# Performance work log

Hardware: AMD Instinct MI355X
Metric: run time of the kernel (lower is better)

## Reference

```python
import jax, jax.numpy as jnp
import numpy as np

VOCAB = 100000; D = 300; F_NUM = 768
M = 64; N = 16
SURF_L = 4; CTX_L = 50; DOC_L = 100; BODY_L = 200
HEADS = 5


def _conv_relu_avg(x, W, b):
    # x: [B, L, D] tokens-embedded; conv1d (valid) + relu + global avgpool -> [B, F]
    y = jax.lax.conv_general_dilated(x.transpose(0, 2, 1), W, (1,), 'VALID',
                                     dimension_numbers=('NCH', 'OIH', 'NCH'))
    return jax.nn.relu(y + b[None, :, None]).mean(axis=2)


def _mha(q, k, v, num_heads=HEADS):
    # split-head scaled dot-product attention (no learned projections), q:[Lq,D] k,v:[Lk,D]
    Lq, Dm = q.shape
    hd = Dm // num_heads
    qh = q.reshape(Lq, num_heads, hd).transpose(1, 0, 2)
    kh = k.reshape(k.shape[0], num_heads, hd).transpose(1, 0, 2)
    vh = v.reshape(v.shape[0], num_heads, hd).transpose(1, 0, 2)
    att = jax.nn.softmax(jnp.einsum('hqd,hkd->hqk', qh, kh) * (1.0 / np.sqrt(hd)), axis=-1)
    out = jnp.einsum('hqk,hkd->hqd', att, vh)
    return out.transpose(1, 0, 2).reshape(Lq, Dm)


def _cos(a, b, eps=1e-6):
    na = jnp.maximum(jnp.sqrt((a * a).sum(-1)), eps)
    nb = jnp.maximum(jnp.sqrt((b * b).sum(-1)), eps)
    return (a * b).sum(-1) / (na * nb)


def setup_inputs() -> dict:
    key = jax.random.key(0)
    ks = jax.random.split(key, 20)
    inp = {}
    inp['mention_entity'] = jnp.ones((M, N), dtype=jnp.int32)
    inp['m'] = M
    inp['n'] = N
    inp['mention_vec'] = jax.random.randint(ks[0], (M, SURF_L), 0, VOCAB)
    inp['context_vec'] = jax.random.randint(ks[1], (M, CTX_L), 0, VOCAB)
    inp['doc_vec'] = jax.random.randint(ks[2], (DOC_L,), 0, VOCAB)
    inp['title_vec'] = jax.random.normal(ks[3], (N, F_NUM), dtype=jnp.float32)
    inp['body_vec'] = jax.random.randint(ks[4], (N, BODY_L), 0, VOCAB)
    inp['sfeats'] = jnp.zeros((N, 1), dtype=jnp.float32)
    inp['m2c_prior'] = jax.random.uniform(ks[5], (N,), dtype=jnp.float32)
    inp['men2cands'] = jax.random.randint(ks[6], (M, N), 0, VOCAB)
    inp['contexts_ids'] = jax.random.randint(ks[7], (M, CTX_L), 0, VOCAB)
    inp['hand_features'] = jax.random.uniform(ks[8], (N, 1), dtype=jnp.float32)
    inp['bert_doc_vec'] = jax.random.normal(ks[9], (1, F_NUM), dtype=jnp.float32)
    # learned parameters
    inp['embed_table'] = jax.random.normal(ks[10], (VOCAB, D), dtype=jnp.float32) * 0.1
    inp['conv_ms_w'] = jax.random.normal(ks[11], (F_NUM, D, 2), dtype=jnp.float32) * 0.05
    inp['conv_ms_b'] = jnp.zeros((F_NUM,), dtype=jnp.float32)
    inp['conv_mc_w'] = jax.random.normal(ks[12], (F_NUM, D, 5), dtype=jnp.float32) * 0.05
    inp['conv_mc_b'] = jnp.zeros((F_NUM,), dtype=jnp.float32)
    inp['layer_local_w'] = jax.random.normal(ks[13], (7,), dtype=jnp.float32) * 0.3
    inp['layer_local_b'] = jnp.zeros((), dtype=jnp.float32)
    inp['att_w1'] = jax.random.normal(ks[14], (600, 300), dtype=jnp.float32) * 0.05
    inp['att_b1'] = jnp.zeros((300,), dtype=jnp.float32)
    inp['att_w2'] = jax.random.normal(ks[15], (300, 1), dtype=jnp.float32) * 0.05
    inp['att_b2'] = jnp.zeros((), dtype=jnp.float32)
    return inp


def reference(mention_entity, m, n, mention_vec, context_vec, doc_vec, title_vec,
              body_vec, sfeats, m2c_prior, men2cands, contexts_ids, hand_features,
              bert_doc_vec, embed_table, conv_ms_w, conv_ms_b, conv_mc_w, conv_mc_b,
              layer_local_w, layer_local_b, att_w1, att_b1, att_w2, att_b2):
    # per-mention conv features (vectorized over all mentions at once)
    ms = _conv_relu_avg(embed_table[mention_vec], conv_ms_w, conv_ms_b)   # [M,768]
    mc = _conv_relu_avg(embed_table[context_vec], conv_mc_w, conv_mc_b)   # [M,768]
    md = bert_doc_vec[0]                                                  # [768]
    doc_emb = embed_table[doc_vec]                                        # [100,300]
    body_emb = embed_table[body_vec]                                      # [N,200,300]

    # per-candidate cross attention doc<->body, max-pooled over query positions
    att_d_b = jax.vmap(lambda b: _mha(doc_emb, b, b).max(axis=0))(body_emb)          # [N,300]
    att_b_d = jax.vmap(lambda b: _mha(b, doc_emb, doc_emb).max(axis=0))(body_emb)    # [N,300]
    comb = jnp.concatenate([att_d_b, att_b_d], axis=-1)                              # [N,600]
    att_score = jax.nn.sigmoid(jax.nn.relu(comb @ att_w1 + att_b1) @ att_w2 + att_b2)[:, 0]  # [N]

    # LocalCtxAttRanker: candidate-vs-context attention score
    ctx_emb = embed_table[contexts_ids]                                   # [M,50,300]
    cand_emb = embed_table[men2cands]                                     # [M,N,300]
    tok = jnp.einsum('mnd,mtd->mnt', cand_emb, ctx_emb)                   # [M,N,50]
    p = jax.nn.softmax(tok.max(axis=1), axis=-1)                          # [M,50]
    ctxv = jnp.einsum('mt,mtd->md', p, ctx_emb)                           # [M,300]
    local_att = jnp.einsum('mnd,md->mn', cand_emb, ctxv)                  # [M,N]

    cos_st = _cos(ms[:, None, :], title_vec[None, :, :])                  # [M,N]
    cos_dt = _cos(md[None, :], title_vec)                                 # [N]
    cos_ct = _cos(mc[:, None, :], title_vec[None, :, :])                  # [M,N]

    Mm = ms.shape[0]
    bc = lambda v: jnp.broadcast_to(v[None, :], (Mm, v.shape[0]))
    # feature order matches torch.cat((hand_fea, prior, localAtt, attScore, C_score))
    feats = jnp.stack([bc(hand_features[:, 0]), bc(m2c_prior), local_att,
                       bc(att_score), cos_st, bc(cos_dt), cos_ct], axis=-1)  # [M,N,7]
    score = feats @ layer_local_w + layer_local_b                         # [M,N]

    # per-mention standardization (unbiased std, as torch.std), softmax and uniform renorm
    mu = score.mean(axis=1, keepdims=True)
    sd = score.std(axis=1, keepdims=True, ddof=1)
    z = (score - mu) / sd
    sm = jax.nn.softmax(z, axis=1)
    zmin = z.min(axis=1, keepdims=True)
    zmax = z.max(axis=1, keepdims=True)
    u = (z + 1.0 - zmin) / (zmax - zmin)
    u = u / u.sum(axis=1, keepdims=True)
    return (z, sm, u)
```

## Files before the change

kernel.cpp:

```cpp
#include <hip/hip_runtime.h>

#define MM 64
#define NN 16
#define DDIM 300
#define FNUM 768
#define SURF_LL 4
#define CTX_LL 50
#define DOC_LL 100
#define BODY_LL 200
#define NHEADS 5
#define HDIM 60

#define GM 2944
#define GK 1536
#define GN 768

typedef unsigned short u16;
typedef unsigned int u32;
typedef __attribute__((ext_vector_type(8))) short short8;
typedef __attribute__((ext_vector_type(4))) float f32x4;

#define OFF_MSG    0
#define OFF_CTX2G  76800
#define OFF_CANDG  1036800
#define OFF_MS     1344000
#define OFF_MC     1393152
#define OFF_PV0    1442304
#define OFF_PV1    1461504
#define OFF_ASC    1495104
#define OFF_LATT   1495120
#define OFF_ABF    1496144
#define OFF_WTMC   (OFF_ABF + GM*GK/2)
#define OFF_WTMS   (OFF_WTMC + GN*GK/2)

__device__ __forceinline__ u16 f2bf(float x) {
  union { float f; u32 u; } v; v.f = x;
  u32 r = v.u + 0x7FFFu + ((v.u >> 16) & 1u);
  return (u16)(r >> 16);
}

__global__ __launch_bounds__(256) void mega_prep_kernel(
    const float* __restrict__ embed,
    const int* __restrict__ mention_vec,
    const int* __restrict__ context_vec,
    const int* __restrict__ contexts_ids,
    const int* __restrict__ men2cands,
    const float* __restrict__ Wmc,
    const float* __restrict__ Wms,
    float* __restrict__ dst, float* __restrict__ mc,
    float* __restrict__ att_logit,
    u32* __restrict__ Abf, u32* __restrict__ WTmc, float* __restrict__ WTms) {
  int bid = blockIdx.x;
  if (bid < 5250) {
    int e = bid * 256 + threadIdx.x;
    int row = e / DDIM;
    int col = e - row * DDIM;
    int tok;
    if (row < 256)       tok = mention_vec[row];
    else if (row < 3456) tok = contexts_ids[row - 256];
    else                 tok = men2cands[row - 3456];
    dst[e] = embed[(size_t)tok * DDIM + col];
  } else if (bid < 5442) {
    mc[(bid - 5250) * 256 + threadIdx.x] = 0.f;
  } else if (bid == 5442) {
    if (threadIdx.x < NN) att_logit[threadIdx.x] = 0.f;
  } else if (bid < 14275) {
    int idx = (bid - 5443) * 256 + threadIdx.x;
    int r = idx / (GK / 2);
    int kp = idx - r * (GK / 2);
    int k = kp * 2;
    int m = r / 46, t = r - m * 46;
    u32 out = 0;
#pragma unroll
    for (int j = 0; j < 2; j++) {
      int kj = k + j;
      u16 h = 0;
      if (kj < 1500) {
        int tap = kj / 300;
        int d = kj - tap * 300;
        int tok = context_vec[m * CTX_LL + t + tap];
        h = f2bf(embed[(size_t)tok * DDIM + d]);
      }
      out |= (u32)h << (16 * j);
    }
    Abf[idx] = out;
  } else if (bid < 16579) {
    int idx = (bid - 14275) * 256 + threadIdx.x;
    int n = idx / (GK / 2);
    int kp = idx - n * (GK / 2);
    int k = kp * 2;
    u32 out = 0;
#pragma unroll
    for (int j = 0; j < 2; j++) {
      int kj = k + j;
      u16 h = 0;
      if (kj < 1500) {
        int tap = kj / 300;
        int d = kj - tap * 300;
        h = f2bf(Wmc[(size_t)n * 1500 + d * 5 + tap]);
      }
      out |= (u32)h << (16 * j);
    }
    WTmc[idx] = out;
  } else {
    int idx = (bid - 16579) * 256 + threadIdx.x;
    int k = idx / FNUM;
    int f = idx - k * FNUM;
    WTms[idx] = Wms[(size_t)f * 600 + k];
  }
}

__global__ __launch_bounds__(256) void conv_gemm_kernel(
    const u16* __restrict__ A,
    const u16* __restrict__ B,
    const float* __restrict__ bias,
    float* __restrict__ mc) {
  int bn = blockIdx.x, bm = blockIdx.y;
  __shared__ u16 As[64][72];
  __shared__ u16 Bs[64][72];
  int tid = threadIdx.x;
  int w = tid >> 6, lane = tid & 63;
  int wr = w >> 1, wc = w & 1;
  int lg = lane >> 4, lm = lane & 15;
  f32x4 acc[2][2];
#pragma unroll
  for (int i = 0; i < 2; i++)
#pragma unroll
    for (int j = 0; j < 2; j++) acc[i][j] = (f32x4)0.f;
  int c0row = tid >> 3, ck = (tid & 7) * 8;
  const u16* Ag = A + (size_t)(bm * 64) * GK;
  const u16* Bg = B + (size_t)(bn * 64) * GK;
  for (int kt = 0; kt < GK / 64; kt++) {
    int k0 = kt * 64;
    uint4 av0 = *(const uint4*)(Ag + (size_t)c0row * GK + k0 + ck);
    uint4 av1 = *(const uint4*)(Ag + (size_t)(c0row + 32) * GK + k0 + ck);
    uint4 bv0 = *(const uint4*)(Bg + (size_t)c0row * GK + k0 + ck);
    uint4 bv1 = *(const uint4*)(Bg + (size_t)(c0row + 32) * GK + k0 + ck);
    __syncthreads();
    *(uint4*)&As[c0row][ck] = av0;
    *(uint4*)&As[c0row + 32][ck] = av1;
    *(uint4*)&Bs[c0row][ck] = bv0;
    *(uint4*)&Bs[c0row + 32][ck] = bv1;
    __syncthreads();
#pragma unroll
    for (int kk = 0; kk < 2; kk++) {
      short8 af0 = *(const short8*)&As[wr * 32 + lm][kk * 32 + lg * 8];
      short8 af1 = *(const short8*)&As[wr * 32 + 16 + lm][kk * 32 + lg * 8];
      short8 bf0 = *(const short8*)&Bs[wc * 32 + lm][kk * 32 + lg * 8];
      short8 bf1 = *(const short8*)&Bs[wc * 32 + 16 + lm][kk * 32 + lg * 8];
      acc[0][0] = __builtin_amdgcn_mfma_f32_16x16x32_bf16(af0, bf0, acc[0][0], 0, 0, 0);
      acc[0][1] = __builtin_amdgcn_mfma_f32_16x16x32_bf16(af0, bf1, acc[0][1], 0, 0, 0);
      acc[1][0] = __builtin_amdgcn_mfma_f32_16x16x32_bf16(af1, bf0, acc[1][0], 0, 0, 0);
      acc[1][1] = __builtin_amdgcn_mfma_f32_16x16x32_bf16(af1, bf1, acc[1][1], 0, 0, 0);
    }
  }
#pragma unroll
  for (int mf = 0; mf < 2; mf++)
#pragma unroll
    for (int nf = 0; nf < 2; nf++) {
      int col = bn * 64 + wc * 32 + nf * 16 + lm;
      float bb = bias[col];
      int base = bm * 64 + wr * 32 + mf * 16 + lg * 4;
      int mcur = base / 46;
      float s = 0.f;
#pragma unroll
      for (int r = 0; r < 4; r++) {
        float v = fmaxf(acc[mf][nf][r] + bb, 0.f) * (1.0f / 46.0f);
        int mm = (base + r) / 46;
        if (mm != mcur) { atomicAdd(&mc[mcur * FNUM + col], s); s = 0.f; mcur = mm; }
        s += v;
      }
      atomicAdd(&mc[mcur * FNUM + col], s);
    }
}

__device__ __forceinline__ void conv_ms_body(
    const float* __restrict__ msg, const float* __restrict__ WT,
    const float* __restrict__ B, float* __restrict__ ms, int b) {
  int m = b / 3, fi = b - m * 3;
  int f = fi * 256 + threadIdx.x;
  const float* x = msg + m * SURF_LL * DDIM;
  float a0 = 0.f, a1 = 0.f, a2 = 0.f;
  for (int d = 0; d < DDIM; d++) {
    float v0 = x[d], v1 = x[DDIM + d], v2 = x[2 * DDIM + d], v3 = x[3 * DDIM + d];
    float wA = WT[(size_t)(2 * d) * FNUM + f];
    float wB = WT[(size_t)(2 * d + 1) * FNUM + f];
    a0 += v0 * wA + v1 * wB;
    a1 += v1 * wA + v2 * wB;
    a2 += v2 * wA + v3 * wB;
  }
  float bb = B[f];
  float r = fmaxf(a0 + bb, 0.f) + fmaxf(a1 + bb, 0.f) + fmaxf(a2 + bb, 0.f);
  ms[m * FNUM + f] = r * (1.0f / 3.0f);
}

template <int DIR>
__device__ __forceinline__ void scores_pv_body(
    const float* __restrict__ embed, const int* __restrict__ doc_vec,
    const int* __restrict__ body_vec, float* __restrict__ pvp, int b,
    float* __restrict__ smem) {
  constexpr int Lq = DIR ? 200 : 100;
  constexpr int Lk = DIR ? 100 : 200;
  constexpr int KPL = DIR ? 2 : 4;
  constexpr int NQT = DIR ? 7 : 4;
  constexpr int NHALF = DIR ? 1 : 2;
  int qt = b / 80;
  int rem = b - qt * 80;
  int n = rem / 5, h = rem - n * 5;
  const int* qids = DIR ? body_vec + n * BODY_LL : doc_vec;
  const int* kids = DIR ? doc_vec : body_vec + n * BODY_LL;
  float* Ks = smem;
  float* Qs = smem + 12400;
  float* Pl = smem + 12400;
  float* red = smem + 15600;
  for (int idx = threadIdx.x; idx < Lk * 15; idx += 256) {
    int r = idx / 15, c = idx - r * 15;
    float4 v = *(const float4*)(embed + (size_t)kids[r] * DDIM + h * HDIM + c * 4);
    float* dp = Ks + r * 62 + c * 4;
    dp[0] = v.x; dp[1] = v.y; dp[2] = v.z; dp[3] = v.w;
  }
  for (int idx = threadIdx.x; idx < 32 * 15; idx += 256) {
    int r = idx / 15, c = idx - r * 15;
    int q = qt * 32 + r; if (q >= Lq) q = Lq - 1;
    float4 v = *(const float4*)(embed + (size_t)qids[q] * DDIM + h * HDIM + c * 4);
    float* dp = Qs + r * 64 + c * 4;
    dp[0] = v.x; dp[1] = v.y; dp[2] = v.z; dp[3] = v.w;
  }
  __syncthreads();
  int w = threadIdx.x >> 6, lane = threadIdx.x & 63;
  int kcl[KPL];
#pragma unroll
  for (int j = 0; j < KPL; j++) {
    int kk = lane + 64 * j; kcl[j] = (kk < Lk) ? kk : (Lk - 1);
  }
  float acc[8][KPL];
#pragma unroll
  for (int i = 0; i < 8; i++)
#pragma unroll
    for (int j = 0; j < KPL; j++) acc[i][j] = 0.f;
  for (int d = 0; d < HDIM; d += 4) {
    float2 kva[KPL], kvb[KPL];
#pragma unroll
    for (int j = 0; j < KPL; j++) {
      kva[j] = *(const float2*)&Ks[kcl[j] * 62 + d];
      kvb[j] = *(const float2*)&Ks[kcl[j] * 62 + d + 2];
    }
#pragma unroll
    for (int i = 0; i < 8; i++) {
      float4 qv = *(const float4*)&Qs[(w * 8 + i) * 64 + d];
#pragma unroll
      for (int j = 0; j < KPL; j++)
        acc[i][j] += qv.x * kva[j].x + qv.y * kva[j].y +
                     qv.z * kvb[j].x + qv.w * kvb[j].y;
    }
  }
  const float scale = 0.12909944487358056f;
#pragma unroll
  for (int i = 0; i < 8; i++) {
    float mx = -1e30f;
#pragma unroll
    for (int j = 0; j < KPL; j++)
      if (lane + 64 * j < Lk) mx = fmaxf(mx, acc[i][j]);
#pragma unroll
    for (int o = 32; o >= 1; o >>= 1) mx = fmaxf(mx, __shfl_xor(mx, o));
    float mxs = mx * scale;
    float p[KPL];
    float s = 0.f;
#pragma unroll
    for (int j = 0; j < KPL; j++) {
      p[j] = (lane + 64 * j < Lk) ? __expf(acc[i][j] * scale - mxs) : 0.f;
      s += p[j];
    }
#pragma unroll
    for (int o = 32; o >= 1; o >>= 1) s += __shfl_xor(s, o);
    float inv = 1.0f / s;
#pragma unroll
    for (int j = 0; j < KPL; j++) acc[i][j] = p[j] * inv;
  }
  __syncthreads();
  float o[8];
#pragma unroll
  for (int i = 0; i < 8; i++) o[i] = 0.f;
  int dl = (lane < HDIM) ? lane : (HDIM - 1);
#pragma unroll
  for (int half = 0; half < NHALF; half++) {
    int kbase = half * 100;
#pragma unroll
    for (int j = 0; j < KPL; j++) {
      int kk = lane + 64 * j;
      int rel = kk - kbase;
      if (rel >= 0 && rel < 100 && kk < Lk) {
#pragma unroll
        for (int i = 0; i < 8; i++)
          Pl[(w * 8 + i) * 100 + rel] = acc[i][j];
      }
    }
    for (int k4 = 0; k4 < 25; k4++) {
      int k = kbase + k4 * 4;
      float kv0 = Ks[(k + 0) * 62 + dl];
      float kv1 = Ks[(k + 1) * 62 + dl];
      float kv2 = Ks[(k + 2) * 62 + dl];
      float kv3 = Ks[(k + 3) * 62 + dl];
#pragma unroll
      for (int i = 0; i < 8; i++) {
        float4 pq = *(const float4*)&Pl[(w * 8 + i) * 100 + k4 * 4];
        o[i] += pq.x * kv0 + pq.y * kv1 + pq.z * kv2 + pq.w * kv3;
      }
    }
  }
  float omax = -1e30f;
#pragma unroll
  for (int i = 0; i < 8; i++) {
    int q = qt * 32 + w * 8 + i;
    if (q < Lq) omax = fmaxf(omax, o[i]);
  }
  red[w * 64 + lane] = omax;
  __syncthreads();
  if (threadIdx.x < 64 && lane < HDIM) {
    float m4 = fmaxf(fmaxf(red[0 * 64 + lane], red[1 * 64 + lane]),
                     fmaxf(red[2 * 64 + lane], red[3 * 64 + lane]));
    pvp[((size_t)(n * NHEADS + h) * NQT + qt) * HDIM + lane] = m4;
  }
}

__device__ __forceinline__ void tokctxv_body(
    const float* __restrict__ candg, const float* __restrict__ ctx2g,
    float* __restrict__ local_att, int m, float* __restrict__ smem) {
  float* cand  = smem;
  float* ctx   = smem + 4800;
  float* tokb  = smem + 9600;
  float* tkmx  = smem + 9872;
  float* pp    = smem + 9936;
  float* sctxv = smem + 10000;
  int tid = threadIdx.x;
  for (int i = tid; i < NN * DDIM; i += 256)
    cand[i] = candg[(size_t)m * NN * DDIM + i];
  int nI = tid >> 4, tt = tid & 15;
  for (int tile = 0; tile < 4; tile++) {
    int cbase = tile * 16;
    __syncthreads();
    for (int i = tid; i < 16 * DDIM; i += 256) {
      int rr = i / DDIM, cc = i - rr * DDIM;
      int t = cbase + rr;
      ctx[rr * DDIM + cc] = (t < CTX_LL) ? ctx2g[(size_t)(m * CTX_LL + t) * DDIM + cc] : 0.f;
    }
    __syncthreads();
    const float4* ca = (const float4*)(cand + nI * DDIM);
    const float4* cb = (const float4*)(ctx + tt * DDIM);
    float dsum = 0.f;
#pragma unroll
    for (int c = 0; c < 75; c++) {
      float4 a = ca[c], b = cb[c];
      dsum += a.x * b.x + a.y * b.y + a.z * b.z + a.w * b.w;
    }
    tokb[nI * 17 + tt] = dsum;
    __syncthreads();
    if (tid < 16) {
      float mx = -1e30f;
      for (int nn = 0; nn < NN; nn++) mx = fmaxf(mx, tokb[nn * 17 + tid]);
      int t = cbase + tid;
      if (t < CTX_LL) tkmx[t] = mx;
    }
  }
  __syncthreads();
  if (tid < 64) {
    float v = (tid < CTX_LL) ? tkmx[tid] : -1e30f;
    float mx = v;
#pragma unroll
    for (int o = 32; o >= 1; o >>= 1) mx = fmaxf(mx, __shfl_xor(mx, o));
    float e = (tid < CTX_LL) ? expf(v - mx) : 0.f;
    float s = e;
#pragma unroll
    for (int o = 32; o >= 1; o >>= 1) s += __shfl_xor(s, o);
    pp[tid] = e / s;
  }
  __syncthreads();
  for (int d = tid; d < DDIM; d += 256) {
    float acc = 0.f;
    for (int t = 0; t < CTX_LL; t++)
      acc += pp[t] * ctx2g[(size_t)(m * CTX_LL + t) * DDIM + d];
    sctxv[d] = acc;
  }
  __syncthreads();
  int j = tid & 15;
  float dd = 0.f;
  for (int i = j; i < DDIM; i += 16) dd += cand[nI * DDIM + i] * sctxv[i];
#pragma unroll
  for (int o = 8; o >= 1; o >>= 1) dd += __shfl_xor(dd, o);
  if (j == 0) local_att[m * NN + nI] = dd;
}

__global__ __launch_bounds__(256) void mega_mid_kernel(
    const float* __restrict__ embed,
    const int* __restrict__ doc_vec,
    const int* __restrict__ body_vec,
    const float* __restrict__ msg,
    const float* __restrict__ WTms,
    const float* __restrict__ Bms,
    const float* __restrict__ candg,
    const float* __restrict__ ctx2g,
    float* __restrict__ ms,
    float* __restrict__ pv0,
    float* __restrict__ pv1,
    float* __restrict__ local_att) {
  __shared__ float smem[15856];
  int bid = blockIdx.x;
  if (bid < 192) {
    conv_ms_body(msg, WTms, Bms, ms, bid);
  } else if (bid < 512) {
    scores_pv_body<0>(embed, doc_vec, body_vec, pv0, bid - 192, smem);
  } else if (bid < 1072) {
    scores_pv_body<1>(embed, doc_vec, body_vec, pv1, bid - 512, smem);
  } else {
    tokctxv_body(candg, ctx2g, local_att, bid - 1072, smem);
  }
}

__global__ __launch_bounds__(256) void mlp_kernel(
    const float* __restrict__ pv0, const float* __restrict__ pv1,
    const float* __restrict__ w1, const float* __restrict__ b1,
    const float* __restrict__ w2,
    float* __restrict__ att_logit) {
  int bid = blockIdx.x;
  int n = bid / 5, jc = bid - n * 5;
  int tid = threadIdx.x;
  __shared__ float comb[600];
  __shared__ float partial[4][64];
  for (int idx = tid; idx < 600; idx += 256) {
    int side = idx >= 300;
    int pos = idx - side * 300;
    int h = pos / 60, d = pos - h * 60;
    float mx = -1e30f;
    if (!side) {
#pragma unroll
      for (int pt = 0; pt < 4; pt++)
        mx = fmaxf(mx, pv0[(size_t)((n * NHEADS + h) * 4 + pt) * HDIM + d]);
    } else {
#pragma unroll
      for (int pt = 0; pt < 7; pt++)
        mx = fmaxf(mx, pv1[(size_t)((n * NHEADS + h) * 7 + pt) * HDIM + d]);
    }
    comb[idx] = mx;
  }
  __syncthreads();
  int w = tid >> 6, lane = tid & 63;
  int jl = (lane < 60) ? lane : 59;
  int jg = jc * 60 + jl;
  float acc = 0.f;
  for (int k = w; k < 600; k += 4)
    acc += comb[k] * w1[(size_t)k * 300 + jg];
  partial[w][lane] = acc;
  __syncthreads();
  if (tid < 64) {
    float hv = partial[0][lane] + partial[1][lane] +
               partial[2][lane] + partial[3][lane];
    float hj = fmaxf(hv + b1[jg], 0.f) * w2[jg];
    if (lane >= 60) hj = 0.f;
#pragma unroll
    for (int o = 32; o >= 1; o >>= 1) hj += __shfl_xor(hj, o);
    if (lane == 0) atomicAdd(&att_logit[n], hj);
  }
}

__global__ __launch_bounds__(256) void final_kernel(
    const float* __restrict__ ms,
    const float* __restrict__ mc,
    const float* __restrict__ title,
    const float* __restrict__ bert,
    const float* __restrict__ att_logit,
    const float* __restrict__ b2,
    const float* __restrict__ m2c_prior,
    const float* __restrict__ hand,
    const float* __restrict__ local_att,
    const float* __restrict__ w7,
    const float* __restrict__ b7,
    float* __restrict__ out) {
  int m = blockIdx.x, tid = threadIdx.x;
  __shared__ float sms[FNUM], smc[FNUM], smd[FNUM];
  __shared__ float snorm[3], sscore[16], wred[3][4];
  for (int i = tid; i < FNUM; i += 256) {
    sms[i] = ms[m * FNUM + i];
    smc[i] = mc[m * FNUM + i];
    smd[i] = bert[i];
  }
  __syncthreads();
  float p1 = 0.f, p2 = 0.f, p3 = 0.f;
  for (int i = tid; i < FNUM; i += 256) {
    float a = sms[i], b = smc[i], c = smd[i];
    p1 += a * a; p2 += b * b; p3 += c * c;
  }
#pragma unroll
  for (int o = 32; o >= 1; o >>= 1) {
    p1 += __shfl_xor(p1, o); p2 += __shfl_xor(p2, o); p3 += __shfl_xor(p3, o);
  }
  int wid = tid >> 6, lane = tid & 63;
  if (lane == 0) { wred[0][wid] = p1; wred[1][wid] = p2; wred[2][wid] = p3; }
  __syncthreads();
  if (tid == 0) {
    snorm[0] = fmaxf(sqrtf(wred[0][0] + wred[0][1] + wred[0][2] + wred[0][3]), 1e-6f);
    snorm[1] = fmaxf(sqrtf(wred[1][0] + wred[1][1] + wred[1][2] + wred[1][3]), 1e-6f);
    snorm[2] = fmaxf(sqrtf(wred[2][0] + wred[2][1] + wred[2][2] + wred[2][3]), 1e-6f);
  }
  __syncthreads();
  int nI = tid >> 4, j = tid & 15;
  float d1 = 0.f, d2 = 0.f, d3 = 0.f, d4 = 0.f;
  for (int i = j; i < FNUM; i += 16) {
    float t = title[nI * FNUM + i];
    d1 += sms[i] * t; d2 += smc[i] * t; d3 += smd[i] * t; d4 += t * t;
  }
#pragma unroll
  for (int o = 8; o >= 1; o >>= 1) {
    d1 += __shfl_xor(d1, o); d2 += __shfl_xor(d2, o);
    d3 += __shfl_xor(d3, o); d4 += __shfl_xor(d4, o);
  }
  if (j == 0) {
    float nt = fmaxf(sqrtf(d4), 1e-6f);
    float cos_st = d1 / (snorm[0] * nt);
    float cos_ct = d2 / (snorm[1] * nt);
    float cos_dt = d3 / (snorm[2] * nt);
    float asc = 1.0f / (1.0f + expf(-(att_logit[nI] + b2[0])));
    float score = hand[nI] * w7[0] + m2c_prior[nI] * w7[1] +
                  local_att[m * NN + nI] * w7[2] + asc * w7[3] +
                  cos_st * w7[4] + cos_dt * w7[5] + cos_ct * w7[6] + b7[0];
    sscore[nI] = score;
  }
  __syncthreads();
  if (tid < 16) {
    float x = sscore[tid];
    float s = x;
#pragma unroll
    for (int o = 8; o >= 1; o >>= 1) s += __shfl_xor(s, o);
    float mu = s * (1.0f / 16.0f);
    float dv = (x - mu) * (x - mu);
    float vs = dv;
#pragma unroll
    for (int o = 8; o >= 1; o >>= 1) vs += __shfl_xor(vs, o);
    float sd = sqrtf(vs * (1.0f / 15.0f));
    float z = (x - mu) / sd;
    float zm = z;
#pragma unroll
    for (int o = 8; o >= 1; o >>= 1) zm = fmaxf(zm, __shfl_xor(zm, o));
    float e = expf(z - zm);
    float es = e;
#pragma unroll
    for (int o = 8; o >= 1; o >>= 1) es += __shfl_xor(es, o);
    float sm = e / es;
    float zmin = z;
#pragma unroll
    for (int o = 8; o >= 1; o >>= 1) zmin = fminf(zmin, __shfl_xor(zmin, o));
    float u0 = (z + 1.0f - zmin) / (zm - zmin);
    float us = u0;
#pragma unroll
    for (int o = 8; o >= 1; o >>= 1) us += __shfl_xor(us, o);
    float u = u0 / us;
    out[m * NN + tid] = z;
    out[MM * NN + m * NN + tid] = sm;
    out[2 * MM * NN + m * NN + tid] = u;
  }
}

extern "C" void kernel_launch(void* const* d_in, const int* in_sizes, int n_in,
                              void* d_out, int out_size, void* d_ws, size_t ws_size,
                              hipStream_t stream) {
  const int*   mention_vec   = (const int*)d_in[3];
  const int*   context_vec   = (const int*)d_in[4];
  const int*   doc_vec       = (const int*)d_in[5];
  const float* title_vec     = (const float*)d_in[6];
  const int*   body_vec      = (const int*)d_in[7];
  const float* m2c_prior     = (const float*)d_in[9];
  const int*   men2cands     = (const int*)d_in[10];
  const int*   contexts_ids  = (const int*)d_in[11];
  const float* hand_features = (const float*)d_in[12];
  const float* bert_doc_vec  = (const float*)d_in[13];
  const float* embed_table   = (const float*)d_in[14];
  const float* conv_ms_w     = (const float*)d_in[15];
  const float* conv_ms_b     = (const float*)d_in[16];
  const float* conv_mc_w     = (const float*)d_in[17];
  const float* conv_mc_b     = (const float*)d_in[18];
  const float* layer_local_w = (const float*)d_in[19];
  const float* layer_local_b = (const float*)d_in[20];
  const float* att_w1        = (const float*)d_in[21];
  const float* att_b1        = (const float*)d_in[22];
  const float* att_w2        = (const float*)d_in[23];
  const float* att_b2        = (const float*)d_in[24];

  float* ws     = (float*)d_ws;
  float* msg    = ws + OFF_MSG;
  float* ctx2g  = ws + OFF_CTX2G;
  float* candg  = ws + OFF_CANDG;
  float* ms     = ws + OFF_MS;
  float* mc     = ws + OFF_MC;
  float* pv0    = ws + OFF_PV0;
  float* pv1    = ws + OFF_PV1;
  float* att_lg = ws + OFF_ASC;
  float* latt   = ws + OFF_LATT;
  u16*   Abf    = (u16*)(ws + OFF_ABF);
  u16*   WTmc   = (u16*)(ws + OFF_WTMC);
  float* WTms   = ws + OFF_WTMS;
  float* out    = (float*)d_out;

  mega_prep_kernel<<<dim3(18379), dim3(256), 0, stream>>>(
      embed_table, mention_vec, context_vec, contexts_ids, men2cands,
      conv_mc_w, conv_ms_w, ws, mc, att_lg, (u32*)Abf, (u32*)WTmc, WTms);
  conv_gemm_kernel<<<dim3(GN / 64, GM / 64), dim3(256), 0, stream>>>(
      Abf, WTmc, conv_mc_b, mc);
  mega_mid_kernel<<<dim3(1136), dim3(256), 0, stream>>>(
      embed_table, doc_vec, body_vec, msg, WTms, conv_ms_b, candg, ctx2g,
      ms, pv0, pv1, latt);
  mlp_kernel<<<dim3(80), dim3(256), 0, stream>>>(
      pv0, pv1, att_w1, att_b1, att_w2, att_lg);
  final_kernel<<<dim3(MM), dim3(256), 0, stream>>>(
      ms, mc, title_vec, bert_doc_vec, att_lg, att_b2, m2c_prior,
      hand_features, latt, layer_local_w, layer_local_b, out);
}
```

Baseline: 399.1 us.

## Stream K tiles with online softmax and shrink shared memory in mid kernel

Restructures the doc/body attention block to process keys in 100-row tiles using an online (flash-style) softmax, with P·V computed via readlane broadcasts instead of staging probabilities in shared memory. The candidate embeddings in tokctxv are now read directly from global memory instead of being copied into LDS. Together these roughly halve the shared-memory footprint and add a launch-bounds hint of 4 blocks per CU, aiming to raise occupancy. The cost is extra syncs and rescaling work per tile, serialized readlane loops, and uncached global reads of cand.

```diff
diff --git a/kernel.cpp b/kernel.cpp
--- a/kernel.cpp
+++ b/kernel.cpp
@@ -37,6 +37,10 @@
   union { float f; u32 u; } v; v.f = x;
   u32 r = v.u + 0x7FFFu + ((v.u >> 16) & 1u);
   return (u16)(r >> 16);
+}
+
+__device__ __forceinline__ float rdlane(float x, int l) {
+  return __uint_as_float(__builtin_amdgcn_readlane(__float_as_uint(x), l));
 }
 
 __global__ __launch_bounds__(256) void mega_prep_kernel(
@@ -200,25 +204,16 @@
     const int* __restrict__ body_vec, float* __restrict__ pvp, int b,
     float* __restrict__ smem) {
   constexpr int Lq = DIR ? 200 : 100;
-  constexpr int Lk = DIR ? 100 : 200;
-  constexpr int KPL = DIR ? 2 : 4;
+  constexpr int NT = DIR ? 1 : 2;
   constexpr int NQT = DIR ? 7 : 4;
-  constexpr int NHALF = DIR ? 1 : 2;
   int qt = b / 80;
   int rem = b - qt * 80;
   int n = rem / 5, h = rem - n * 5;
   const int* qids = DIR ? body_vec + n * BODY_LL : doc_vec;
   const int* kids = DIR ? doc_vec : body_vec + n * BODY_LL;
   float* Ks = smem;
-  float* Qs = smem + 12400;
-  float* Pl = smem + 12400;
-  float* red = smem + 15600;
-  for (int idx = threadIdx.x; idx < Lk * 15; idx += 256) {
-    int r = idx / 15, c = idx - r * 15;
-    float4 v = *(const float4*)(embed + (size_t)kids[r] * DDIM + h * HDIM + c * 4);
-    float* dp = Ks + r * 62 + c * 4;
-    dp[0] = v.x; dp[1] = v.y; dp[2] = v.z; dp[3] = v.w;
-  }
+  float* Qs = smem + 6200;
+  float* red = smem + 8248;
   for (int idx = threadIdx.x; idx < 32 * 15; idx += 256) {
     int r = idx / 15, c = idx - r * 15;
     int q = qt * 32 + r; if (q >= Lq) q = Lq - 1;
@@ -226,93 +221,76 @@
     float* dp = Qs + r * 64 + c * 4;
     dp[0] = v.x; dp[1] = v.y; dp[2] = v.z; dp[3] = v.w;
   }
-  __syncthreads();
   int w = threadIdx.x >> 6, lane = threadIdx.x & 63;
-  int kcl[KPL];
-#pragma unroll
-  for (int j = 0; j < KPL; j++) {
-    int kk = lane + 64 * j; kcl[j] = (kk < Lk) ? kk : (Lk - 1);
-  }
-  float acc[8][KPL];
-#pragma unroll
-  for (int i = 0; i < 8; i++)
-#pragma unroll
-    for (int j = 0; j < KPL; j++) acc[i][j] = 0.f;
-  for (int d = 0; d < HDIM; d += 4) {
-    float2 kva[KPL], kvb[KPL];
-#pragma unroll
-    for (int j = 0; j < KPL; j++) {
-      kva[j] = *(const float2*)&Ks[kcl[j] * 62 + d];
-      kvb[j] = *(const float2*)&Ks[kcl[j] * 62 + d + 2];
+  int dl = (lane < HDIM) ? lane : (HDIM - 1);
+  const float scale = 0.12909944487358056f;
+  float mrun[8], srun[8], O[8];
+#pragma unroll
+  for (int i = 0; i < 8; i++) { mrun[i] = -1e30f; srun[i] = 0.f; O[i] = 0.f; }
+  int kc0 = lane;
+  int kc1 = (lane + 64 < 100) ? lane + 64 : 99;
+  bool v1ok = (lane + 64 < 100);
+  for (int kt = 0; kt < NT; kt++) {
+    if (kt > 0) __syncthreads();
+    for (int idx = threadIdx.x; idx < 100 * 15; idx += 256) {
+      int r = idx / 15, c = idx - r * 15;
+      float4 v = *(const float4*)(embed + (size_t)kids[kt * 100 + r] * DDIM + h * HDIM + c * 4);
+      float* dp = Ks + r * 62 + c * 4;
+      dp[0] = v.x; dp[1] = v.y; dp[2] = v.z; dp[3] = v.w;
+    }
+    __syncthreads();
+    float acc[8][2];
+#pragma unroll
+    for (int i = 0; i < 8; i++) { acc[i][0] = 0.f; acc[i][1] = 0.f; }
+    for (int d = 0; d < HDIM; d += 4) {
+      float2 a0 = *(const float2*)&Ks[kc0 * 62 + d];
+      float2 b0 = *(const float2*)&Ks[kc0 * 62 + d + 2];
+      float2 a1 = *(const float2*)&Ks[kc1 * 62 + d];
+      float2 b1 = *(const float2*)&Ks[kc1 * 62 + d + 2];
+#pragma unroll
+      for (int i = 0; i < 8; i++) {
+        float4 qv = *(const float4*)&Qs[(w * 8 + i) * 64 + d];
+        acc[i][0] += qv.x * a0.x + qv.y * a0.y + qv.z * b0.x + qv.w * b0.y;
+        acc[i][1] += qv.x * a1.x + qv.y * a1.y + qv.z * b1.x + qv.w * b1.y;
+      }
     }
 #pragma unroll
     for (int i = 0; i < 8; i++) {
-      float4 qv = *(const float4*)&Qs[(w * 8 + i) * 64 + d];
-#pragma unroll
-      for (int j = 0; j < KPL; j++)
-        acc[i][j] += qv.x * kva[j].x + qv.y * kva[j].y +
-                     qv.z * kvb[j].x + qv.w * kvb[j].y;
-    }
-  }
-  const float scale = 0.12909944487358056f;
-#pragma unroll
-  for (int i = 0; i < 8; i++) {
-    float mx = -1e30f;
-#pragma unroll
-    for (int j = 0; j < KPL; j++)
-      if (lane + 64 * j < Lk) mx = fmaxf(mx, acc[i][j]);
-#pragma unroll
-    for (int o = 32; o >= 1; o >>= 1) mx = fmaxf(mx, __shfl_xor(mx, o));
-    float mxs = mx * scale;
-    float p[KPL];
-    float s = 0.f;
-#pragma unroll
-    for (int j = 0; j < KPL; j++) {
-      p[j] = (lane + 64 * j < Lk) ? __expf(acc[i][j] * scale - mxs) : 0.f;
-      s += p[j];
-    }
-#pragma unroll
-    for (int o = 32; o >= 1; o >>= 1) s += __shfl_xor(s, o);
-    float inv = 1.0f / s;
-#pragma unroll
-    for (int j = 0; j < KPL; j++) acc[i][j] = p[j] * inv;
-  }
-  __syncthreads();
-  float o[8];
-#pragma unroll
-  for (int i = 0; i < 8; i++) o[i] = 0.f;
-  int dl = (lane < HDIM) ? lane : (HDIM - 1);
-#pragma unroll
-  for (int half = 0; half < NHALF; half++) {
-    int kbase = half * 100;
-#pragma unroll
-    for (int j = 0; j < KPL; j++) {
-      int kk = lane + 64 * j;
-      int rel = kk - kbase;
-      if (rel >= 0 && rel < 100 && kk < Lk) {
-#pragma unroll
-        for (int i = 0; i < 8; i++)
-          Pl[(w * 8 + i) * 100 + rel] = acc[i][j];
-      }
-    }
-    for (int k4 = 0; k4 < 25; k4++) {
-      int k = kbase + k4 * 4;
-      float kv0 = Ks[(k + 0) * 62 + dl];
-      float kv1 = Ks[(k + 1) * 62 + dl];
-      float kv2 = Ks[(k + 2) * 62 + dl];
-      float kv3 = Ks[(k + 3) * 62 + dl];
-#pragma unroll
-      for (int i = 0; i < 8; i++) {
-        float4 pq = *(const float4*)&Pl[(w * 8 + i) * 100 + k4 * 4];
-        o[i] += pq.x * kv0 + pq.y * kv1 + pq.z * kv2 + pq.w * kv3;
-      }
+      float v0 = acc[i][0] * scale;
+      float v1 = v1ok ? acc[i][1] * scale : -1e30f;
+      float tm = fmaxf(v0, v1);
+#pragma unroll
+      for (int o = 32; o >= 1; o >>= 1) tm = fmaxf(tm, __shfl_xor(tm, o));
+      float mn = fmaxf(mrun[i], tm);
+      float fsc = __expf(mrun[i] - mn);
+      float p0 = __expf(v0 - mn);
+      float p1 = v1ok ? __expf(v1 - mn) : 0.f;
+      float ts = p0 + p1;
+#pragma unroll
+      for (int o = 32; o >= 1; o >>= 1) ts += __shfl_xor(ts, o);
+      srun[i] = srun[i] * fsc + ts;
+      mrun[i] = mn;
+      O[i] *= fsc;
+      acc[i][0] = p0; acc[i][1] = p1;
+    }
+#pragma unroll 4
+    for (int k = 0; k < 64; k++) {
+      float vk = Ks[k * 62 + dl];
+#pragma unroll
+      for (int i = 0; i < 8; i++) O[i] += rdlane(acc[i][0], k) * vk;
+    }
+#pragma unroll 4
+    for (int k = 64; k < 100; k++) {
+      float vk = Ks[k * 62 + dl];
+#pragma unroll
+      for (int i = 0; i < 8; i++) O[i] += rdlane(acc[i][1], k - 64) * vk;
     }
   }
   float omax = -1e30f;
 #pragma unroll
   for (int i = 0; i < 8; i++) {
     int q = qt * 32 + w * 8 + i;
-    if (q < Lq) omax = fmaxf(omax, o[i]);
+    if (q < Lq) omax = fmaxf(omax, O[i] / srun[i]);
   }
   red[w * 64 + lane] = omax;
   __syncthreads();
@@ -326,16 +304,14 @@
 __device__ __forceinline__ void tokctxv_body(
     const float* __restrict__ candg, const float* __restrict__ ctx2g,
     float* __restrict__ local_att, int m, float* __restrict__ smem) {
-  float* cand  = smem;
-  float* ctx   = smem + 4800;
-  float* tokb  = smem + 9600;
-  float* tkmx  = smem + 9872;
-  float* pp    = smem + 9936;
-  float* sctxv = smem + 10000;
+  float* ctx   = smem;
+  float* tokb  = smem + 4800;
+  float* tkmx  = smem + 5072;
+  float* pp    = smem + 5136;
+  float* sctxv = smem + 5200;
   int tid = threadIdx.x;
-  for (int i = tid; i < NN * DDIM; i += 256)
-    cand[i] = candg[(size_t)m * NN * DDIM + i];
   int nI = tid >> 4, tt = tid & 15;
+  const float* cand = candg + (size_t)m * NN * DDIM;
   for (int tile = 0; tile < 4; tile++) {
     int cbase = tile * 16;
     __syncthreads();
@@ -390,7 +366,7 @@
   if (j == 0) local_att[m * NN + nI] = dd;
 }
 
-__global__ __launch_bounds__(256) void mega_mid_kernel(
+__global__ __launch_bounds__(256, 4) void mega_mid_kernel(
     const float* __restrict__ embed,
     const int* __restrict__ doc_vec,
     const int* __restrict__ body_vec,
@@ -403,7 +379,7 @@
     float* __restrict__ pv0,
     float* __restrict__ pv1,
     float* __restrict__ local_att) {
-  __shared__ float smem[15856];
+  __shared__ float smem[8504];
   int bid = blockIdx.x;
   if (bid < 192) {
     conv_ms_body(msg, WTms, Bms, ms, bid);
```

Measured after the change: 439.3 us. +10.1%, slower.

## Merge conv GEMM blocks into the mid-stage mega kernel launch

Applied to the files above, without the earlier changes.

Turns the standalone conv GEMM kernel into a device body and dispatches its 552 tiles as extra blocks of the mid-stage mega kernel, so one launch replaces two. This removes a kernel launch and the serialization between the GEMM and the independent mid-stage work, letting them run concurrently. In exchange the GEMM now uses the mega kernel's large shared-memory allocation, which may lower occupancy for those blocks.

```diff
diff --git a/kernel.cpp b/kernel.cpp
--- a/kernel.cpp
+++ b/kernel.cpp
@@ -110,14 +110,14 @@
   }
 }
 
-__global__ __launch_bounds__(256) void conv_gemm_kernel(
+__device__ __forceinline__ void conv_gemm_body(
     const u16* __restrict__ A,
     const u16* __restrict__ B,
     const float* __restrict__ bias,
-    float* __restrict__ mc) {
-  int bn = blockIdx.x, bm = blockIdx.y;
-  __shared__ u16 As[64][72];
-  __shared__ u16 Bs[64][72];
+    float* __restrict__ mc, int g, float* __restrict__ smem) {
+  int bn = g % (GN / 64), bm = g / (GN / 64);
+  u16* As = (u16*)smem;
+  u16* Bs = (u16*)(smem + 2304);
   int tid = threadIdx.x;
   int w = tid >> 6, lane = tid & 63;
   int wr = w >> 1, wc = w & 1;
@@ -137,17 +137,17 @@
     uint4 bv0 = *(const uint4*)(Bg + (size_t)c0row * GK + k0 + ck);
     uint4 bv1 = *(const uint4*)(Bg + (size_t)(c0row + 32) * GK + k0 + ck);
     __syncthreads();
-    *(uint4*)&As[c0row][ck] = av0;
-    *(uint4*)&As[c0row + 32][ck] = av1;
-    *(uint4*)&Bs[c0row][ck] = bv0;
-    *(uint4*)&Bs[c0row + 32][ck] = bv1;
+    *(uint4*)&As[c0row * 72 + ck] = av0;
+    *(uint4*)&As[(c0row + 32) * 72 + ck] = av1;
+    *(uint4*)&Bs[c0row * 72 + ck] = bv0;
+    *(uint4*)&Bs[(c0row + 32) * 72 + ck] = bv1;
     __syncthreads();
 #pragma unroll
     for (int kk = 0; kk < 2; kk++) {
-      short8 af0 = *(const short8*)&As[wr * 32 + lm][kk * 32 + lg * 8];
-      short8 af1 = *(const short8*)&As[wr * 32 + 16 + lm][kk * 32 + lg * 8];
-      short8 bf0 = *(const short8*)&Bs[wc * 32 + lm][kk * 32 + lg * 8];
-      short8 bf1 = *(const short8*)&Bs[wc * 32 + 16 + lm][kk * 32 + lg * 8];
+      short8 af0 = *(const short8*)&As[(wr * 32 + lm) * 72 + kk * 32 + lg * 8];
+      short8 af1 = *(const short8*)&As[(wr * 32 + 16 + lm) * 72 + kk * 32 + lg * 8];
+      short8 bf0 = *(const short8*)&Bs[(wc * 32 + lm) * 72 + kk * 32 + lg * 8];
+      short8 bf1 = *(const short8*)&Bs[(wc * 32 + 16 + lm) * 72 + kk * 32 + lg * 8];
       acc[0][0] = __builtin_amdgcn_mfma_f32_16x16x32_bf16(af0, bf0, acc[0][0], 0, 0, 0);
       acc[0][1] = __builtin_amdgcn_mfma_f32_16x16x32_bf16(af0, bf1, acc[0][1], 0, 0, 0);
       acc[1][0] = __builtin_amdgcn_mfma_f32_16x16x32_bf16(af1, bf0, acc[1][0], 0, 0, 0);
@@ -399,7 +399,11 @@
     const float* __restrict__ Bms,
     const float* __restrict__ candg,
     const float* __restrict__ ctx2g,
+    const u16* __restrict__ Abf,
+    const u16* __restrict__ WTmc,
+    const float* __restrict__ Bmc,
     float* __restrict__ ms,
+    float* __restrict__ mc,
     float* __restrict__ pv0,
     float* __restrict__ pv1,
     float* __restrict__ local_att) {
@@ -411,8 +415,10 @@
     scores_pv_body<0>(embed, doc_vec, body_vec, pv0, bid - 192, smem);
   } else if (bid < 1072) {
     scores_pv_body<1>(embed, doc_vec, body_vec, pv1, bid - 512, smem);
+  } else if (bid < 1136) {
+    tokctxv_body(candg, ctx2g, local_att, bid - 1072, smem);
   } else {
-    tokctxv_body(candg, ctx2g, local_att, bid - 1072, smem);
+    conv_gemm_body(Abf, WTmc, Bmc, mc, bid - 1136, smem);
   }
 }
 
@@ -602,11 +608,9 @@
   mega_prep_kernel<<<dim3(18379), dim3(256), 0, stream>>>(
       embed_table, mention_vec, context_vec, contexts_ids, men2cands,
       conv_mc_w, conv_ms_w, ws, mc, att_lg, (u32*)Abf, (u32*)WTmc, WTms);
-  conv_gemm_kernel<<<dim3(GN / 64, GM / 64), dim3(256), 0, stream>>>(
-      Abf, WTmc, conv_mc_b, mc);
-  mega_mid_kernel<<<dim3(1136), dim3(256), 0, stream>>>(
+  mega_mid_kernel<<<dim3(1688), dim3(256), 0, stream>>>(
       embed_table, doc_vec, body_vec, msg, WTms, conv_ms_b, candg, ctx2g,
-      ms, pv0, pv1, latt);
+      Abf, WTmc, conv_mc_b, ms, mc, pv0, pv1, latt);
   mlp_kernel<<<dim3(80), dim3(256), 0, stream>>>(
       pv0, pv1, att_w1, att_b1, att_w2, att_lg);
   final_kernel<<<dim3(MM), dim3(256), 0, stream>>>(
```

Result: faster. 375.8 us (-5.8%).
